# Optimization experiments

Hardware: AMD Instinct MI355X
Metric: run time of the kernel (lower is better)

## Reference

```python
import jax, jax.numpy as jnp
import numpy as np
import math

B, T, D = 32, 336, 512
H = 8
HD = D // H
SEG_PER_DAY = 24
DAYS_PER_CYCLE = 7
NEG_INF = -1e30


def setup_inputs() -> dict:
    key = jax.random.key(0)
    ks = jax.random.split(key, 7)
    s = 1.0 / math.sqrt(D)
    x = jax.random.normal(ks[0], (B, T, D), dtype=jnp.float32)
    Wq = jax.random.uniform(ks[1], (D, D), minval=-s, maxval=s, dtype=jnp.float32)
    Wk = jax.random.uniform(ks[2], (D, D), minval=-s, maxval=s, dtype=jnp.float32)
    Wv = jax.random.uniform(ks[3], (D, D), minval=-s, maxval=s, dtype=jnp.float32)
    so = 1.0 / math.sqrt(2 * D)
    Wo = jax.random.uniform(ks[4], (2 * D, D), minval=-so, maxval=so, dtype=jnp.float32)
    bo = jax.random.uniform(ks[5], (D,), minval=-so, maxval=so, dtype=jnp.float32)
    random_bias = jax.random.normal(ks[6], (2, T, T), dtype=jnp.float32) * 0.01
    return {"x": x, "Wq": Wq, "Wk": Wk, "Wv": Wv, "Wo": Wo, "bo": bo,
            "random_bias": random_bias}


def reference(x, Wq, Wk, Wv, Wo, bo, random_bias):
    b, t, d = x.shape
    q = (x @ Wq).reshape(b, t, H, HD).transpose(0, 2, 1, 3)  # [b,h,t,hd]
    k = (x @ Wk).reshape(b, t, H, HD).transpose(0, 2, 1, 3)
    v = (x @ Wv).reshape(b, t, H, HD).transpose(0, 2, 1, 3)

    idx = jnp.arange(t)
    hour_ids = idx % SEG_PER_DAY
    day_ids = (idx // SEG_PER_DAY) % DAYS_PER_CYCLE
    hour_adj = hour_ids[:, None] == hour_ids[None, :]   # [t,t] bool
    day_adj = day_ids[:, None] == day_ids[None, :]

    # base QK^T scores computed once, reused for both granularities
    base = jnp.einsum('bhqd,bhkd->bhqk', q, k) / math.sqrt(HD)  # [b,h,t,t]

    def graph_attn(adj, bias):
        scores = base + bias[None, None]                      # additive bias
        scores = jnp.where(adj[None, None], scores, NEG_INF)  # periodic mask
        attn = jax.nn.softmax(scores, axis=-1)
        return jnp.einsum('bhqk,bhkd->bhqd', attn, v)

    hour_out = graph_attn(hour_adj, random_bias[0, :t, :t])
    day_out = graph_attn(day_adj, random_bias[1, :t, :t])

    hour_out = hour_out.transpose(0, 2, 1, 3).reshape(b, t, d)
    day_out = day_out.transpose(0, 2, 1, 3).reshape(b, t, d)
    combined = jnp.concatenate([hour_out, day_out], axis=-1)  # [b,t,2d]
    return combined @ Wo + bo
```

## Files before the change

### kernel.cpp

```cpp
#include <hip/hip_runtime.h>


typedef __attribute__((ext_vector_type(8))) __bf16 bf16x8;
typedef __attribute__((ext_vector_type(8))) unsigned short u16x8;
typedef __attribute__((ext_vector_type(4))) float f32x4;

__device__ __forceinline__ unsigned short f2bf(float f) {
  union { float f; unsigned u; } v; v.f = f;
  unsigned r = v.u + 0x7fffu + ((v.u >> 16) & 1u);
  return (unsigned short)(r >> 16);
}

__device__ __forceinline__ void load_lds16(const void* g, void* l) {
  __builtin_amdgcn_global_load_lds(
      (const __attribute__((address_space(1))) void*)g,
      (__attribute__((address_space(3))) void*)l, 16, 0, 0);
}

template <bool OUT_BF16, int BM>
__global__ __launch_bounds__(256) void gemm_bt(
    const unsigned short* __restrict__ A, const unsigned short* __restrict__ Bt,
    void* __restrict__ Cv, const float* __restrict__ bias, int M, int N, int K) {
  constexpr int MR = BM / 32;
  constexpr int AIT = BM / 32;
  __shared__ __align__(16) unsigned short As[BM * 64];
  __shared__ __align__(16) unsigned short Bs[128 * 64];
  const int tid = threadIdx.x;
  const int lane = tid & 63;
  const int wid = tid >> 6;
  const int ntile = N >> 7;

  const int cpx = gridDim.x >> 3;
  const int bid = (blockIdx.x & 7) * cpx + (blockIdx.x >> 3);

  const int bx = bid % ntile;
  const int by = bid / ntile;
  const long row0 = (long)by * BM;
  const long col0 = (long)bx << 7;
  const int wr = (wid >> 1) * (BM >> 1);
  const int wc = (wid & 1) << 6;

  const unsigned short* ag[AIT];
  const unsigned short* bg[4];
  int alofs[AIT], blofs[4];
#pragma unroll
  for (int it = 0; it < AIT; ++it) {
    const int s = tid + (it << 8);
    const int r = s >> 3;
    const int c = s & 7;
    ag[it] = A + (row0 + r) * (long)K + (((c ^ (r & 7)) << 3));
    alofs[it] = s << 4;
  }
#pragma unroll
  for (int it = 0; it < 4; ++it) {
    const int s = tid + (it << 8);
    const int r = s >> 3;
    const int c = s & 7;
    bg[it] = Bt + (col0 + r) * (long)K + (((c ^ (r & 7)) << 3));
    blofs[it] = s << 4;
  }

  f32x4 acc[MR][4];
  const f32x4 zero = {0.f, 0.f, 0.f, 0.f};
#pragma unroll
  for (int m = 0; m < MR; ++m)
#pragma unroll
    for (int n = 0; n < 4; ++n) acc[m][n] = zero;

  const int fr = lane & 15;
  const int grp = lane >> 4;
  const int sw = fr & 7;

  for (int kk = 0; kk < K; kk += 64) {
#pragma unroll
    for (int it = 0; it < AIT; ++it)
      load_lds16(ag[it] + kk, (char*)As + alofs[it]);
#pragma unroll
    for (int it = 0; it < 4; ++it)
      load_lds16(bg[it] + kk, (char*)Bs + blofs[it]);
    __syncthreads();
#pragma unroll
    for (int ks = 0; ks < 2; ++ks) {
      const int kc = ks * 4 + grp;
      bf16x8 a[MR], b[4];
#pragma unroll
      for (int m = 0; m < MR; ++m) {
        const int row = wr + m * 16 + fr;
        a[m] = *(const bf16x8*)(const void*)(As + row * 64 + ((kc ^ sw) << 3));
      }
#pragma unroll
      for (int n = 0; n < 4; ++n) {
        const int row = wc + n * 16 + fr;
        b[n] = *(const bf16x8*)(const void*)(Bs + row * 64 + ((kc ^ sw) << 3));
      }
#pragma unroll
      for (int m = 0; m < MR; ++m)
#pragma unroll
        for (int n = 0; n < 4; ++n)
          acc[m][n] = __builtin_amdgcn_mfma_f32_16x16x32_bf16(a[m], b[n], acc[m][n], 0, 0, 0);
    }
    __syncthreads();
  }

  const int orow = (lane >> 4) << 2;
  const int ocol = lane & 15;
#pragma unroll
  for (int m = 0; m < MR; ++m) {
#pragma unroll
    for (int n = 0; n < 4; ++n) {
      const long gcol = col0 + wc + n * 16 + ocol;
      float bv = 0.f;
      if (!OUT_BF16 && bias) bv = bias[gcol];
#pragma unroll
      for (int r = 0; r < 4; ++r) {
        const long grow = row0 + wr + m * 16 + orow + r;
        const float val = acc[m][n][r] + bv;
        if (OUT_BF16)
          ((unsigned short*)Cv)[grow * N + gcol] = f2bf(val);
        else
          ((float*)Cv)[grow * N + gcol] = val;
      }
    }
  }
}

template <int MODE>
__device__ __forceinline__ void attn_body(
    const int cls, const int h, const int b, const int lane,
    const unsigned short* __restrict__ QKV, const float* __restrict__ bias,
    unsigned short* __restrict__ comb, unsigned short* smem) {
  constexpr int NQT = MODE ? 3 : 1;
  constexpr int NKT = MODE ? 3 : 1;
  constexpr int PVK = MODE ? 2 : 1;
  constexpr int MEM = MODE ? 48 : 14;
  constexpr int PLD = MODE ? 72 : 40;
  constexpr int VLD = MODE ? 72 : 40;
  constexpr int PE = 16 * NQT * PLD;
  constexpr int VE = 64 * VLD;

  unsigned short* P_lds = smem;
  unsigned short* Vt = smem + PE;
  const long rowBase = (long)b * 336;

  auto tmap = [&](int i) -> int {
    if (MODE) return 24 * cls + i + ((i < 24) ? 0 : 144);
    return cls + 24 * i;
  };

  {
    const uint4 z4 = {0u, 0u, 0u, 0u};
    uint4* p4 = (uint4*)P_lds;
#pragma unroll
    for (int i = 0; i < PE / 8 / 64 + 1; ++i) {
      const int idx = lane + i * 64;
      if (idx < PE / 8) p4[idx] = z4;
    }
    uint4* v4 = (uint4*)Vt;
#pragma unroll
    for (int i = 0; i < VE / 8 / 64 + 1; ++i) {
      const int idx = lane + i * 64;
      if (idx < VE / 8) v4[idx] = z4;
    }
  }
  __syncthreads();

  {
    const int kloc = lane >> 3;
    const int d0 = (lane & 7) * 8;
    constexpr int NPASS = (MEM + 7) / 8;
#pragma unroll
    for (int p = 0; p < NPASS; ++p) {
      const int k = p * 8 + kloc;
      if (k < MEM) {
        const long off = (rowBase + tmap(k)) * 1536 + 1024 + h * 64 + d0;
        const u16x8 vv = *(const u16x8*)(const void*)(QKV + off);
#pragma unroll
        for (int e = 0; e < 8; ++e) Vt[(d0 + e) * VLD + k] = vv[e];
      }
    }
  }

  const int fr = lane & 15;
  const int kgrp = (lane >> 4) << 3;
  bf16x8 aq[NQT][2], bk[NKT][2];
#pragma unroll
  for (int it = 0; it < NQT; ++it) {
    const int qi = 16 * it + fr;
    const long rq = (rowBase + tmap(qi < MEM ? qi : MEM - 1)) * 1536 + h * 64 + kgrp;
#pragma unroll
    for (int ks = 0; ks < 2; ++ks)
      aq[it][ks] = *(const bf16x8*)(const void*)(QKV + rq + ks * 32);
  }
#pragma unroll
  for (int jt = 0; jt < NKT; ++jt) {
    const int kj = 16 * jt + fr;
    const long rk = (rowBase + tmap(kj < MEM ? kj : MEM - 1)) * 1536 + 512 + h * 64 + kgrp;
#pragma unroll
    for (int ks = 0; ks < 2; ++ks)
      bk[jt][ks] = *(const bf16x8*)(const void*)(QKV + rk + ks * 32);
  }

  f32x4 sacc[NQT][NKT];
  const f32x4 zero = {0.f, 0.f, 0.f, 0.f};
#pragma unroll
  for (int it = 0; it < NQT; ++it)
#pragma unroll
    for (int jt = 0; jt < NKT; ++jt) sacc[it][jt] = zero;
#pragma unroll
  for (int ks = 0; ks < 2; ++ks)
#pragma unroll
    for (int it = 0; it < NQT; ++it)
#pragma unroll
      for (int jt = 0; jt < NKT; ++jt)
        sacc[it][jt] = __builtin_amdgcn_mfma_f32_16x16x32_bf16(aq[it][ks], bk[jt][ks], sacc[it][jt], 0, 0, 0);

  const int rgrp = (lane >> 4) << 2;
#pragma unroll
  for (int it = 0; it < NQT; ++it) {
#pragma unroll
    for (int r = 0; r < 4; ++r) {
      const int row = 16 * it + rgrp + r;
      const int tq = tmap(row < MEM ? row : MEM - 1);
      float sv[NKT];
#pragma unroll
      for (int jt = 0; jt < NKT; ++jt) {
        const int col = 16 * jt + fr;
        const int tk = tmap(col < MEM ? col : MEM - 1);
        sv[jt] = sacc[it][jt][r] * 0.125f + bias[(long)tq * 336 + tk];
        if (MODE == 0 && col >= MEM) sv[jt] = -1e30f;
      }
      float m = sv[0];
#pragma unroll
      for (int jt = 1; jt < NKT; ++jt) m = fmaxf(m, sv[jt]);
#pragma unroll
      for (int d = 1; d < 16; d <<= 1) m = fmaxf(m, __shfl_xor(m, d, 64));
      float e[NKT], sum = 0.f;
#pragma unroll
      for (int jt = 0; jt < NKT; ++jt) { e[jt] = __expf(sv[jt] - m); sum += e[jt]; }
#pragma unroll
      for (int d = 1; d < 16; d <<= 1) sum += __shfl_xor(sum, d, 64);
      const float inv = 1.f / sum;
#pragma unroll
      for (int jt = 0; jt < NKT; ++jt)
        P_lds[row * PLD + 16 * jt + fr] = f2bf(e[jt] * inv);
    }
  }
  __syncthreads();

  f32x4 oacc[NQT][4];
#pragma unroll
  for (int it = 0; it < NQT; ++it)
#pragma unroll
    for (int jt = 0; jt < 4; ++jt) oacc[it][jt] = zero;
#pragma unroll
  for (int ks = 0; ks < PVK; ++ks) {
    bf16x8 pa[NQT], vb[4];
#pragma unroll
    for (int it = 0; it < NQT; ++it)
      pa[it] = *(const bf16x8*)(const void*)(P_lds + (16 * it + fr) * PLD + ks * 32 + kgrp);
#pragma unroll
    for (int jt = 0; jt < 4; ++jt)
      vb[jt] = *(const bf16x8*)(const void*)(Vt + (16 * jt + fr) * VLD + ks * 32 + kgrp);
#pragma unroll
    for (int it = 0; it < NQT; ++it)
#pragma unroll
      for (int jt = 0; jt < 4; ++jt)
        oacc[it][jt] = __builtin_amdgcn_mfma_f32_16x16x32_bf16(pa[it], vb[jt], oacc[it][jt], 0, 0, 0);
  }

  const long colBase = (MODE ? 512 : 0) + h * 64;
#pragma unroll
  for (int it = 0; it < NQT; ++it) {
#pragma unroll
    for (int r = 0; r < 4; ++r) {
      const int row = 16 * it + rgrp + r;
      if (row < MEM) {
        const long base = (rowBase + tmap(row)) * 1024 + colBase;
#pragma unroll
        for (int jt = 0; jt < 4; ++jt)
          comb[base + 16 * jt + fr] = f2bf(oacc[it][jt][r]);
      }
    }
  }
}

__global__ __launch_bounds__(64) void attn_all(
    const unsigned short* __restrict__ QKV, const float* __restrict__ rb,
    unsigned short* __restrict__ comb) {
  __shared__ __align__(16) unsigned short smem[8064];
  const int lane = threadIdx.x & 63;
  const int bi = blockIdx.x;
  if (bi < 6144) {
    const int c = bi % 24;
    const int h = (bi / 24) & 7;
    const int b = bi / (24 * 8);
    attn_body<0>(c, h, b, lane, QKV, rb, comb, smem);
  } else {
    const int di = bi - 6144;
    const int dc = di % 7;
    const int h = (di / 7) & 7;
    const int b = di / 56;
    attn_body<1>(dc, h, b, lane, QKV, rb + 336 * 336, comb, smem);
  }
}

__global__ __launch_bounds__(256) void cast_all(
    const float* __restrict__ x, const float* __restrict__ Wq,
    const float* __restrict__ Wk, const float* __restrict__ Wv,
    const float* __restrict__ Wo, unsigned short* __restrict__ xb,
    unsigned short* __restrict__ WqkvT, unsigned short* __restrict__ WoT) {
  const int g0 = blockIdx.x * 256 + threadIdx.x;
  const int gsz = gridDim.x * 256;
  for (int i = g0; i < 1376256; i += gsz) {
    const float4 v = ((const float4*)x)[i];
    ushort4 o;
    o.x = f2bf(v.x); o.y = f2bf(v.y); o.z = f2bf(v.z); o.w = f2bf(v.w);
    ((ushort4*)xb)[i] = o;
  }
  for (int idx = g0; idx < 1536 * 512; idx += gsz) {
    const int n = idx >> 9, k = idx & 511;
    const float* W = (n < 512) ? Wq : ((n < 1024) ? Wk : Wv);
    WqkvT[idx] = f2bf(W[k * 512 + (n & 511)]);
  }
  for (int idx = g0; idx < 512 * 1024; idx += gsz) {
    const int n = idx >> 10, k = idx & 1023;
    WoT[idx] = f2bf(Wo[k * 512 + n]);
  }
}

extern "C" void kernel_launch(void* const* d_in, const int* in_sizes, int n_in,
                              void* d_out, int out_size, void* d_ws, size_t ws_size,
                              hipStream_t stream) {
  (void)in_sizes; (void)n_in; (void)out_size; (void)ws_size;
  const float* x  = (const float*)d_in[0];
  const float* Wq = (const float*)d_in[1];
  const float* Wk = (const float*)d_in[2];
  const float* Wv = (const float*)d_in[3];
  const float* Wo = (const float*)d_in[4];
  const float* bo = (const float*)d_in[5];
  const float* rb = (const float*)d_in[6];

  char* ws = (char*)d_ws;
  unsigned short* xbf   = (unsigned short*)(ws + 0);
  unsigned short* WqkvT = (unsigned short*)(ws + 11010048);
  unsigned short* WoT   = (unsigned short*)(ws + 12582912);
  unsigned short* QKVb  = (unsigned short*)(ws + 13631488);
  unsigned short* comb  = (unsigned short*)(ws + 46661632);

  cast_all<<<2048, 256, 0, stream>>>(x, Wq, Wk, Wv, Wo, xbf, WqkvT, WoT);

  gemm_bt<true, 128><<<84 * 12, 256, 0, stream>>>(xbf, WqkvT, QKVb, nullptr, 10752, 1536, 512);

  attn_all<<<6144 + 1792, 64, 0, stream>>>(QKVb, rb, comb);

  gemm_bt<false, 64><<<168 * 4, 256, 0, stream>>>(comb, WoT, d_out, bo, 10752, 512, 1024);
}
```

Measured before the change: 85.28 us.

## Double-buffer LDS in GEMM and use 64-row tiles for QKV projection

```diff
diff --git a/kernel.cpp b/kernel.cpp
--- a/kernel.cpp
+++ b/kernel.cpp
@@ -17,14 +17,12 @@
       (__attribute__((address_space(3))) void*)l, 16, 0, 0);
 }
 
-template <bool OUT_BF16, int BM>
+template <bool OUT_BF16>
 __global__ __launch_bounds__(256) void gemm_bt(
     const unsigned short* __restrict__ A, const unsigned short* __restrict__ Bt,
     void* __restrict__ Cv, const float* __restrict__ bias, int M, int N, int K) {
-  constexpr int MR = BM / 32;
-  constexpr int AIT = BM / 32;
-  __shared__ __align__(16) unsigned short As[BM * 64];
-  __shared__ __align__(16) unsigned short Bs[128 * 64];
+  __shared__ __align__(16) unsigned short As[2 * 64 * 64];
+  __shared__ __align__(16) unsigned short Bs[2 * 128 * 64];
   const int tid = threadIdx.x;
   const int lane = tid & 63;
   const int wid = tid >> 6;
@@ -35,20 +33,20 @@
 
   const int bx = bid % ntile;
   const int by = bid / ntile;
-  const long row0 = (long)by * BM;
+  const long row0 = (long)by << 6;
   const long col0 = (long)bx << 7;
-  const int wr = (wid >> 1) * (BM >> 1);
+  const int wr = (wid >> 1) << 5;
   const int wc = (wid & 1) << 6;
 
-  const unsigned short* ag[AIT];
+  const unsigned short* ag[2];
   const unsigned short* bg[4];
-  int alofs[AIT], blofs[4];
-#pragma unroll
-  for (int it = 0; it < AIT; ++it) {
+  int alofs[2], blofs[4];
+#pragma unroll
+  for (int it = 0; it < 2; ++it) {
     const int s = tid + (it << 8);
     const int r = s >> 3;
     const int c = s & 7;
-    ag[it] = A + (row0 + r) * (long)K + (((c ^ (r & 7)) << 3));
+    ag[it] = A + (row0 + r) * (long)K + ((c ^ (r & 7)) << 3);
     alofs[it] = s << 4;
   }
 #pragma unroll
@@ -56,14 +54,14 @@
     const int s = tid + (it << 8);
     const int r = s >> 3;
     const int c = s & 7;
-    bg[it] = Bt + (col0 + r) * (long)K + (((c ^ (r & 7)) << 3));
+    bg[it] = Bt + (col0 + r) * (long)K + ((c ^ (r & 7)) << 3);
     blofs[it] = s << 4;
   }
 
-  f32x4 acc[MR][4];
+  f32x4 acc[2][4];
   const f32x4 zero = {0.f, 0.f, 0.f, 0.f};
 #pragma unroll
-  for (int m = 0; m < MR; ++m)
+  for (int m = 0; m < 2; ++m)
 #pragma unroll
     for (int n = 0; n < 4; ++n) acc[m][n] = zero;
 
@@ -71,41 +69,58 @@
   const int grp = lane >> 4;
   const int sw = fr & 7;
 
-  for (int kk = 0; kk < K; kk += 64) {
-#pragma unroll
-    for (int it = 0; it < AIT; ++it)
-      load_lds16(ag[it] + kk, (char*)As + alofs[it]);
-#pragma unroll
-    for (int it = 0; it < 4; ++it)
-      load_lds16(bg[it] + kk, (char*)Bs + blofs[it]);
-    __syncthreads();
+  const int NT = K >> 6;
+
+#pragma unroll
+  for (int it = 0; it < 2; ++it)
+    load_lds16(ag[it], (char*)As + alofs[it]);
+#pragma unroll
+  for (int it = 0; it < 4; ++it)
+    load_lds16(bg[it], (char*)Bs + blofs[it]);
+  __syncthreads();
+
+  int cur = 0;
+  for (int t = 0; t < NT; ++t) {
+    if (t + 1 < NT) {
+      const int kk = (t + 1) << 6;
+      const int nb = cur ^ 1;
+#pragma unroll
+      for (int it = 0; it < 2; ++it)
+        load_lds16(ag[it] + kk, (char*)As + nb * 8192 + alofs[it]);
+#pragma unroll
+      for (int it = 0; it < 4; ++it)
+        load_lds16(bg[it] + kk, (char*)Bs + nb * 16384 + blofs[it]);
+    }
+    const unsigned short* Ab = As + cur * 4096;
+    const unsigned short* Bb = Bs + cur * 8192;
 #pragma unroll
     for (int ks = 0; ks < 2; ++ks) {
       const int kc = ks * 4 + grp;
-      bf16x8 a[MR], b[4];
-#pragma unroll
-      for (int m = 0; m < MR; ++m) {
+      bf16x8 a[2], b[4];
+#pragma unroll
+      for (int m = 0; m < 2; ++m) {
         const int row = wr + m * 16 + fr;
-        a[m] = *(const bf16x8*)(const void*)(As + row * 64 + ((kc ^ sw) << 3));
+        a[m] = *(const bf16x8*)(const void*)(Ab + row * 64 + ((kc ^ sw) << 3));
       }
 #pragma unroll
       for (int n = 0; n < 4; ++n) {
         const int row = wc + n * 16 + fr;
-        b[n] = *(const bf16x8*)(const void*)(Bs + row * 64 + ((kc ^ sw) << 3));
-      }
-#pragma unroll
-      for (int m = 0; m < MR; ++m)
+        b[n] = *(const bf16x8*)(const void*)(Bb + row * 64 + ((kc ^ sw) << 3));
+      }
+#pragma unroll
+      for (int m = 0; m < 2; ++m)
 #pragma unroll
         for (int n = 0; n < 4; ++n)
           acc[m][n] = __builtin_amdgcn_mfma_f32_16x16x32_bf16(a[m], b[n], acc[m][n], 0, 0, 0);
     }
     __syncthreads();
+    cur ^= 1;
   }
 
   const int orow = (lane >> 4) << 2;
   const int ocol = lane & 15;
 #pragma unroll
-  for (int m = 0; m < MR; ++m) {
+  for (int m = 0; m < 2; ++m) {
 #pragma unroll
     for (int n = 0; n < 4; ++n) {
       const long gcol = col0 + wc + n * 16 + ocol;
@@ -349,9 +364,9 @@
 
   cast_all<<<2048, 256, 0, stream>>>(x, Wq, Wk, Wv, Wo, xbf, WqkvT, WoT);
 
-  gemm_bt<true, 128><<<84 * 12, 256, 0, stream>>>(xbf, WqkvT, QKVb, nullptr, 10752, 1536, 512);
+  gemm_bt<true><<<168 * 12, 256, 0, stream>>>(xbf, WqkvT, QKVb, nullptr, 10752, 1536, 512);
 
   attn_all<<<6144 + 1792, 64, 0, stream>>>(QKVb, rb, comb);
 
-  gemm_bt<false, 64><<<168 * 4, 256, 0, stream>>>(comb, WoT, d_out, bo, 10752, 512, 1024);
-}
+  gemm_bt<false><<<168 * 4, 256, 0, stream>>>(comb, WoT, d_out, bo, 10752, 512, 1024);
+}
```

Measured after the change: 84.14 us, median of 2. Within noise of the previous version (-1.3%).
